# Kernel optimization log

Measured on AMD Instinct MI355X. Metric: run time of the kernel, lower is better.

## Reference

```python
import jax, jax.numpy as jnp
import numpy as np

B, N, DN, DT = 1024, 200, 128, 128
M = DN + DN + DT  # model_dim = 384 (node + edge + time dims)


def setup_inputs() -> dict:
    key = jax.random.key(0)
    ks = jax.random.split(key, 10)
    rn = lambda k, s, sc=1.0: jax.random.normal(k, s, jnp.float32) * sc
    return {
        'src': rn(ks[0], (B, DN)),
        'src_t': rn(ks[1], (B, 1, DT)),
        'seq': rn(ks[2], (B, N, DN)),
        'seq_t': rn(ks[3], (B, N, DT)),
        'seq_e': rn(ks[4], (B, N, DN)),
        'mask': jax.random.randint(ks[5], (B, N), 0, 2).astype(bool),
        'shared_attn': rn(ks[6], (1, 2 * M), 0.05),
        'fc_w': rn(ks[7], (M, M), 0.05),
        'ln_g': jnp.ones((M,), jnp.float32),
        'ln_b': jnp.zeros((M,), jnp.float32),
        'agg_fc_w1': rn(ks[8], (2 * DN, M + DN), 0.05),
        'agg_fc_w2': rn(ks[9], (DN, 2 * DN), 0.05),
    }


def _layer_norm(x, g, b, eps=1e-5):
    mu = x.mean(-1, keepdims=True)
    var = ((x - mu) ** 2).mean(-1, keepdims=True)
    return (x - mu) * jax.lax.rsqrt(var + eps) * g + b


def reference(src, src_t, seq, seq_t, seq_e, mask, shared_attn, fc_w, ln_g, ln_b, agg_fc_w1, agg_fc_w2):
    # AttnModel.forward with 'simple' Attention (eval mode: dropout off)
    src_ext = src[:, None, :]                                   # [B,1,DN]
    q = jnp.concatenate([src_ext, jnp.zeros_like(src_ext), src_t], axis=2)  # [B,1,M]
    k = jnp.concatenate([seq, seq_e, seq_t], axis=2)            # [B,N,M]
    # F.linear(cat([q_exp, k_exp], -1), shared_attn) == q.w_q + k.w_k (fused, avoids [B,1,N,2M])
    w = shared_attn[0]
    wq, wk = w[:M], w[M:]
    scores = jnp.einsum('bqd,d->bq', q, wq)[:, :, None] + jnp.einsum('bnd,d->bn', k, wk)[:, None, :]  # [B,1,N]
    scores = jnp.where(mask[:, None, :], -1e10, scores)
    attn = jax.nn.softmax(scores, axis=2)                       # [B,1,N]
    out = jnp.einsum('bqn,bnm->bqm', attn, k)                   # [B,1,M] (v == k)
    out = out @ fc_w.T
    out = _layer_norm(out + q, ln_g, ln_b)
    out = out[:, 0, :]                                          # [B,M]
    attn_w = attn[:, 0, :]                                      # [B,N]
    x = jnp.concatenate([out, src], axis=1)                     # [B, M+DN]
    x = jax.nn.relu(x @ agg_fc_w1.T)                            # [B, 2*DN]
    out = x @ agg_fc_w2.T                                       # [B, DN]
    return out, attn_w
```

## Files before the change

### kernel.cpp

```cpp
#include <hip/hip_runtime.h>


constexpr int B_  = 1024;
constexpr int N_  = 200;
constexpr int DN_ = 128;
constexpr int DT_ = 128;
constexpr int M_  = 384;
constexpr int BDIM = 256;
constexpr int NPW  = N_ / 4;

__device__ __forceinline__ float wave_sum(float v) {
#pragma unroll
    for (int off = 32; off > 0; off >>= 1)
        v += __shfl_xor(v, off, 64);
    return v;
}

__global__ __launch_bounds__(BDIM) void tgnn_kernel(
    const float* __restrict__ src,
    const float* __restrict__ src_t,
    const float* __restrict__ seq,
    const float* __restrict__ seq_t,
    const float* __restrict__ seq_e,
    const int*   __restrict__ mask,
    const float* __restrict__ shared_attn,
    const float* __restrict__ fc_w,
    const float* __restrict__ ln_g,
    const float* __restrict__ ln_b,
    const float* __restrict__ w1,
    const float* __restrict__ w2,
    float* __restrict__ out,
    float* __restrict__ attn_out)
{
    const int b    = blockIdx.x;
    const int tid  = threadIdx.x;
    const int wave = tid >> 6;
    const int lane = tid & 63;
    const int e0   = 2 * lane;
    const int e1   = e0 + 1;

    __shared__ float s_p[N_];
    __shared__ float s_q[M_];
    __shared__ float s_oa[4][M_];
    __shared__ float s_outattn[M_];
    __shared__ float s_y[M_ + DN_];
    __shared__ float s_h[2 * DN_];
    __shared__ float s_red[8];

    if (tid < 128) {
        s_q[tid]       = src[b * DN_ + tid];
        s_q[128 + tid] = 0.0f;
        s_q[256 + tid] = src_t[b * DT_ + tid];
    }

    const float* wq = shared_attn;
    const float* wk = shared_attn + M_;
    const float wk0 = wk[e0],       wk1 = wk[e1];
    const float wk2 = wk[128 + e0], wk3 = wk[128 + e1];
    const float wk4 = wk[256 + e0], wk5 = wk[256 + e1];

    float qpart = src[b * DN_ + e0] * wq[e0]
                + src[b * DN_ + e1] * wq[e1]
                + src_t[b * DT_ + e0] * wq[256 + e0]
                + src_t[b * DT_ + e1] * wq[256 + e1];
    const float qdot = wave_sum(qpart);

    float o0 = 0.f, o1 = 0.f, o2 = 0.f, o3 = 0.f, o4 = 0.f, o5 = 0.f;
    float lsum = 0.f;
    const int n_base = wave * NPW;
    for (int n = n_base; n < n_base + NPW; ++n) {
        const long row = (long)(b * N_ + n);
        const float2 a = *(const float2*)&seq  [row * DN_ + e0];
        const float2 e = *(const float2*)&seq_e[row * DN_ + e0];
        const float2 t = *(const float2*)&seq_t[row * DT_ + e0];
        float part = a.x * wk0 + a.y * wk1
                   + e.x * wk2 + e.y * wk3
                   + t.x * wk4 + t.y * wk5;
        float s = wave_sum(part) + qdot;
        float p = mask[row] ? 0.0f : __expf(s);
        if (lane == 0) s_p[n] = p;
        lsum += p;
        o0 += p * a.x; o1 += p * a.y;
        o2 += p * e.x; o3 += p * e.y;
        o4 += p * t.x; o5 += p * t.y;
    }

    if (lane == 0) s_red[wave] = lsum;
    s_oa[wave][e0]       = o0; s_oa[wave][e1]       = o1;
    s_oa[wave][128 + e0] = o2; s_oa[wave][128 + e1] = o3;
    s_oa[wave][256 + e0] = o4; s_oa[wave][256 + e1] = o5;
    __syncthreads();

    const float Z    = s_red[0] + s_red[1] + s_red[2] + s_red[3];
    const float invZ = 1.0f / Z;

    for (int j = tid; j < M_; j += BDIM)
        s_outattn[j] = (s_oa[0][j] + s_oa[1][j] + s_oa[2][j] + s_oa[3][j]) * invZ;
    for (int n = tid; n < N_; n += BDIM)
        attn_out[b * N_ + n] = s_p[n] * invZ;
    __syncthreads();

    for (int r = 0; r < M_ / 4; ++r) {
        const int i = wave * (M_ / 4) + r;
        const float* row = &fc_w[i * M_];
        float part = 0.f;
#pragma unroll
        for (int m = 0; m < 6; ++m)
            part += s_outattn[lane + 64 * m] * row[lane + 64 * m];
        float v = wave_sum(part);
        if (lane == 0) s_y[i] = v + s_q[i];
    }
    __syncthreads();

    float ls = 0.f, lq = 0.f;
    for (int j = tid; j < M_; j += BDIM) {
        float v = s_y[j];
        ls += v; lq += v * v;
    }
    ls = wave_sum(ls); lq = wave_sum(lq);
    if (lane == 0) { s_red[wave] = ls; s_red[4 + wave] = lq; }
    __syncthreads();
    const float mean = (s_red[0] + s_red[1] + s_red[2] + s_red[3]) * (1.0f / M_);
    const float msq  = (s_red[4] + s_red[5] + s_red[6] + s_red[7]) * (1.0f / M_);
    const float rstd = rsqrtf(msq - mean * mean + 1e-5f);
    for (int j = tid; j < M_; j += BDIM)
        s_y[j] = (s_y[j] - mean) * rstd * ln_g[j] + ln_b[j];
    if (tid < 128)
        s_y[M_ + tid] = s_q[tid];
    __syncthreads();

    for (int r = 0; r < 64; ++r) {
        const int i = wave * 64 + r;
        const float* row = &w1[i * (M_ + DN_)];
        float part = 0.f;
#pragma unroll
        for (int m = 0; m < 8; ++m)
            part += s_y[lane + 64 * m] * row[lane + 64 * m];
        float v = wave_sum(part);
        if (lane == 0) s_h[i] = fmaxf(v, 0.0f);
    }
    __syncthreads();

    for (int r = 0; r < 32; ++r) {
        const int i = wave * 32 + r;
        const float* row = &w2[i * (2 * DN_)];
        float part = 0.f;
#pragma unroll
        for (int m = 0; m < 4; ++m)
            part += s_h[lane + 64 * m] * row[lane + 64 * m];
        float v = wave_sum(part);
        if (lane == 0) out[b * DN_ + i] = v;
    }
}

extern "C" void kernel_launch(void* const* d_in, const int* in_sizes, int n_in,
                              void* d_out, int out_size, void* d_ws, size_t ws_size,
                              hipStream_t stream) {
    const float* src         = (const float*)d_in[0];
    const float* src_t       = (const float*)d_in[1];
    const float* seq         = (const float*)d_in[2];
    const float* seq_t       = (const float*)d_in[3];
    const float* seq_e       = (const float*)d_in[4];
    const int*   mask        = (const int*)  d_in[5];
    const float* shared_attn = (const float*)d_in[6];
    const float* fc_w        = (const float*)d_in[7];
    const float* ln_g        = (const float*)d_in[8];
    const float* ln_b        = (const float*)d_in[9];
    const float* w1          = (const float*)d_in[10];
    const float* w2          = (const float*)d_in[11];

    float* out      = (float*)d_out;
    float* attn_out = (float*)d_out + B_ * DN_;

    tgnn_kernel<<<B_, BDIM, 0, stream>>>(src, src_t, seq, seq_t, seq_e, mask,
                                         shared_attn, fc_w, ln_g, ln_b, w1, w2,
                                         out, attn_out);
}
```

Measured before the change: 426.2 us.

## Batch sequence loads in chunks and switch matvecs to thread-per-row float4

The attention loop now loads 10 rows per wave at once and runs their wave reductions interleaved, so more memory requests are in flight and shuffle latency is overlapped. The three dense matvecs change from wave-per-row with shuffle reductions to thread-per-output-row float4 dot products over shared vectors. Launch bounds now request 4 blocks per SM. The risks are higher register pressure from the chunked arrays, and uncoalesced row-strided global weight reads in the thread-per-row matvecs.

Result: slower. 550.4 us (+29.2%).

```diff
diff --git a/kernel.cpp b/kernel.cpp
--- a/kernel.cpp
+++ b/kernel.cpp
@@ -4,10 +4,10 @@
 constexpr int B_  = 1024;
 constexpr int N_  = 200;
 constexpr int DN_ = 128;
-constexpr int DT_ = 128;
 constexpr int M_  = 384;
 constexpr int BDIM = 256;
 constexpr int NPW  = N_ / 4;
+constexpr int CH   = 10;
 
 __device__ __forceinline__ float wave_sum(float v) {
 #pragma unroll
@@ -16,7 +16,7 @@
     return v;
 }
 
-__global__ __launch_bounds__(BDIM) void tgnn_kernel(
+__global__ __launch_bounds__(BDIM, 4) void tgnn_kernel(
     const float* __restrict__ src,
     const float* __restrict__ src_t,
     const float* __restrict__ seq,
@@ -37,58 +37,75 @@
     const int wave = tid >> 6;
     const int lane = tid & 63;
     const int e0   = 2 * lane;
-    const int e1   = e0 + 1;
 
     __shared__ float s_p[N_];
-    __shared__ float s_q[M_];
+    __shared__ __align__(16) float s_q[M_];
     __shared__ float s_oa[4][M_];
-    __shared__ float s_outattn[M_];
-    __shared__ float s_y[M_ + DN_];
-    __shared__ float s_h[2 * DN_];
+    __shared__ __align__(16) float s_outattn[M_];
+    __shared__ __align__(16) float s_y[M_ + DN_];
+    __shared__ __align__(16) float s_h[2 * DN_];
     __shared__ float s_red[8];
 
     if (tid < 128) {
         s_q[tid]       = src[b * DN_ + tid];
         s_q[128 + tid] = 0.0f;
-        s_q[256 + tid] = src_t[b * DT_ + tid];
+        s_q[256 + tid] = src_t[b * DN_ + tid];
     }
 
     const float* wq = shared_attn;
     const float* wk = shared_attn + M_;
-    const float wk0 = wk[e0],       wk1 = wk[e1];
-    const float wk2 = wk[128 + e0], wk3 = wk[128 + e1];
-    const float wk4 = wk[256 + e0], wk5 = wk[256 + e1];
-
-    float qpart = src[b * DN_ + e0] * wq[e0]
-                + src[b * DN_ + e1] * wq[e1]
-                + src_t[b * DT_ + e0] * wq[256 + e0]
-                + src_t[b * DT_ + e1] * wq[256 + e1];
+    const float wk0 = wk[e0],       wk1 = wk[e0 + 1];
+    const float wk2 = wk[128 + e0], wk3 = wk[128 + e0 + 1];
+    const float wk4 = wk[256 + e0], wk5 = wk[256 + e0 + 1];
+
+    float qpart = src[b * DN_ + e0]     * wq[e0]
+                + src[b * DN_ + e0 + 1] * wq[e0 + 1]
+                + src_t[b * DN_ + e0]     * wq[256 + e0]
+                + src_t[b * DN_ + e0 + 1] * wq[256 + e0 + 1];
     const float qdot = wave_sum(qpart);
 
     float o0 = 0.f, o1 = 0.f, o2 = 0.f, o3 = 0.f, o4 = 0.f, o5 = 0.f;
     float lsum = 0.f;
     const int n_base = wave * NPW;
-    for (int n = n_base; n < n_base + NPW; ++n) {
-        const long row = (long)(b * N_ + n);
-        const float2 a = *(const float2*)&seq  [row * DN_ + e0];
-        const float2 e = *(const float2*)&seq_e[row * DN_ + e0];
-        const float2 t = *(const float2*)&seq_t[row * DT_ + e0];
-        float part = a.x * wk0 + a.y * wk1
-                   + e.x * wk2 + e.y * wk3
-                   + t.x * wk4 + t.y * wk5;
-        float s = wave_sum(part) + qdot;
-        float p = mask[row] ? 0.0f : __expf(s);
-        if (lane == 0) s_p[n] = p;
-        lsum += p;
-        o0 += p * a.x; o1 += p * a.y;
-        o2 += p * e.x; o3 += p * e.y;
-        o4 += p * t.x; o5 += p * t.y;
+    for (int c = 0; c < NPW / CH; ++c) {
+        const int n0 = n_base + c * CH;
+        float2 a[CH], e[CH], t[CH];
+        int mk[CH];
+#pragma unroll
+        for (int j = 0; j < CH; ++j) {
+            const long row = (long)(b * N_ + n0 + j);
+            a[j] = *(const float2*)&seq  [row * DN_ + e0];
+            e[j] = *(const float2*)&seq_e[row * DN_ + e0];
+            t[j] = *(const float2*)&seq_t[row * DN_ + e0];
+            mk[j] = mask[row];
+        }
+        float s[CH];
+#pragma unroll
+        for (int j = 0; j < CH; ++j)
+            s[j] = a[j].x * wk0 + a[j].y * wk1
+                 + e[j].x * wk2 + e[j].y * wk3
+                 + t[j].x * wk4 + t[j].y * wk5;
+#pragma unroll
+        for (int off = 32; off > 0; off >>= 1) {
+#pragma unroll
+            for (int j = 0; j < CH; ++j)
+                s[j] += __shfl_xor(s[j], off, 64);
+        }
+#pragma unroll
+        for (int j = 0; j < CH; ++j) {
+            const float p = mk[j] ? 0.0f : __expf(s[j] + qdot);
+            if (lane == j) s_p[n0 + j] = p;
+            lsum += p;
+            o0 += p * a[j].x; o1 += p * a[j].y;
+            o2 += p * e[j].x; o3 += p * e[j].y;
+            o4 += p * t[j].x; o5 += p * t[j].y;
+        }
     }
 
     if (lane == 0) s_red[wave] = lsum;
-    s_oa[wave][e0]       = o0; s_oa[wave][e1]       = o1;
-    s_oa[wave][128 + e0] = o2; s_oa[wave][128 + e1] = o3;
-    s_oa[wave][256 + e0] = o4; s_oa[wave][256 + e1] = o5;
+    s_oa[wave][e0]           = o0; s_oa[wave][e0 + 1]       = o1;
+    s_oa[wave][128 + e0]     = o2; s_oa[wave][128 + e0 + 1] = o3;
+    s_oa[wave][256 + e0]     = o4; s_oa[wave][256 + e0 + 1] = o5;
     __syncthreads();
 
     const float Z    = s_red[0] + s_red[1] + s_red[2] + s_red[3];
@@ -100,21 +117,23 @@
         attn_out[b * N_ + n] = s_p[n] * invZ;
     __syncthreads();
 
-    for (int r = 0; r < M_ / 4; ++r) {
-        const int i = wave * (M_ / 4) + r;
-        const float* row = &fc_w[i * M_];
-        float part = 0.f;
-#pragma unroll
-        for (int m = 0; m < 6; ++m)
-            part += s_outattn[lane + 64 * m] * row[lane + 64 * m];
-        float v = wave_sum(part);
-        if (lane == 0) s_y[i] = v + s_q[i];
+    const float4* xa = (const float4*)s_outattn;
+    for (int i = tid; i < M_; i += BDIM) {
+        const float4* row = (const float4*)&fc_w[i * M_];
+        float acc = 0.f;
+#pragma unroll
+        for (int j = 0; j < M_ / 4; ++j) {
+            const float4 w = row[j];
+            const float4 x = xa[j];
+            acc += w.x * x.x + w.y * x.y + w.z * x.z + w.w * x.w;
+        }
+        s_y[i] = acc + s_q[i];
     }
     __syncthreads();
 
     float ls = 0.f, lq = 0.f;
     for (int j = tid; j < M_; j += BDIM) {
-        float v = s_y[j];
+        const float v = s_y[j];
         ls += v; lq += v * v;
     }
     ls = wave_sum(ls); lq = wave_sum(lq);
@@ -129,27 +148,31 @@
         s_y[M_ + tid] = s_q[tid];
     __syncthreads();
 
-    for (int r = 0; r < 64; ++r) {
-        const int i = wave * 64 + r;
-        const float* row = &w1[i * (M_ + DN_)];
-        float part = 0.f;
-#pragma unroll
-        for (int m = 0; m < 8; ++m)
-            part += s_y[lane + 64 * m] * row[lane + 64 * m];
-        float v = wave_sum(part);
-        if (lane == 0) s_h[i] = fmaxf(v, 0.0f);
-    }
-    __syncthreads();
-
-    for (int r = 0; r < 32; ++r) {
-        const int i = wave * 32 + r;
-        const float* row = &w2[i * (2 * DN_)];
-        float part = 0.f;
-#pragma unroll
-        for (int m = 0; m < 4; ++m)
-            part += s_h[lane + 64 * m] * row[lane + 64 * m];
-        float v = wave_sum(part);
-        if (lane == 0) out[b * DN_ + i] = v;
+    {
+        const float4* xb = (const float4*)s_y;
+        const float4* row = (const float4*)&w1[tid * (M_ + DN_)];
+        float acc = 0.f;
+#pragma unroll
+        for (int j = 0; j < (M_ + DN_) / 4; ++j) {
+            const float4 w = row[j];
+            const float4 x = xb[j];
+            acc += w.x * x.x + w.y * x.y + w.z * x.z + w.w * x.w;
+        }
+        s_h[tid] = fmaxf(acc, 0.0f);
+    }
+    __syncthreads();
+
+    if (tid < DN_) {
+        const float4* xc = (const float4*)s_h;
+        const float4* row = (const float4*)&w2[tid * (2 * DN_)];
+        float acc = 0.f;
+#pragma unroll
+        for (int j = 0; j < (2 * DN_) / 4; ++j) {
+            const float4 w = row[j];
+            const float4 x = xc[j];
+            acc += w.x * x.x + w.y * x.y + w.z * x.z + w.w * x.w;
+        }
+        out[b * DN_ + tid] = acc;
     }
 }
 
@@ -169,10 +192,10 @@
     const float* w1          = (const float*)d_in[10];
     const float* w2          = (const float*)d_in[11];
 
-    float* out      = (float*)d_out;
+    float* outp     = (float*)d_out;
     float* attn_out = (float*)d_out + B_ * DN_;
 
     tgnn_kernel<<<B_, BDIM, 0, stream>>>(src, src_t, seq, seq_t, seq_e, mask,
                                          shared_attn, fc_w, ln_g, ln_b, w1, w2,
-                                         out, attn_out);
+                                         outp, attn_out);
 }
```
